# Kernel optimization log

Measured on AMD Instinct MI355X. Metric: run time of the kernel, lower is better.

Reference implementation:

```python
import jax, jax.numpy as jnp
import numpy as np

EPS = 1e-12  # matches torch F.normalize default eps

def _l2_normalize(x):
    # F.normalize: x / max(||x||, eps)
    n = jnp.linalg.norm(x, axis=-1, keepdims=True)
    return x / jnp.maximum(n, EPS)

def setup_inputs() -> dict:
    key = jax.random.key(0)
    k1, k2 = jax.random.split(key)
    sat = jax.random.normal(k1, (256, 64, 128), dtype=jnp.float32)   # [b, j, d]
    pano = jax.random.normal(k2, (64, 64, 128), dtype=jnp.float32)   # [a, i, d]
    return {"sat_embeddings_unnormalized": sat,
            "pano_embeddings_unnormalized": pano}

def reference(sat_embeddings_unnormalized, pano_embeddings_unnormalized):
    pano_n = _l2_normalize(pano_embeddings_unnormalized)  # [a, i, d]
    sat_n = _l2_normalize(sat_embeddings_unnormalized)    # [b, j, d]
    # similarity: [a, b, i, j]
    sim = jnp.einsum('aid,bjd->abij', pano_n, sat_n)
    # maxsim: max over sat tokens (j), sum over pano tokens (i) -> [a, b]
    return sim.max(axis=3).sum(axis=2)
```

## Files before the change

### kernel.cpp

```cpp
#include <hip/hip_runtime.h>
#include <hip/hip_bf16.h>


typedef __bf16 bf16x8 __attribute__((ext_vector_type(8)));
typedef float  f32x16 __attribute__((ext_vector_type(16)));
typedef unsigned int u32;

__device__ __forceinline__ void gload16(const void* g, void* l) {
    __builtin_amdgcn_global_load_lds((const __attribute__((address_space(1))) u32*)g,
                                     (__attribute__((address_space(3))) u32*)l, 16, 0, 0);
}

__device__ __forceinline__ unsigned short f2bf_rne(float x) {
    u32 u = __builtin_bit_cast(u32, x);
    return (unsigned short)((u + 0x7FFFu + ((u >> 16) & 1u)) >> 16);
}

__global__ __launch_bounds__(256) void normalize_all(
        const float* __restrict__ sat, const float* __restrict__ pano,
        unsigned short* __restrict__ satN, unsigned short* __restrict__ panoN) {
    int row  = blockIdx.x * 8 + (threadIdx.x >> 5);
    int lane = threadIdx.x & 31;
    const float* src;
    unsigned short* dst;
    if (row < 16384) { src = sat  + (size_t)row * 128;           dst = satN  + (size_t)row * 128; }
    else             { src = pano + (size_t)(row - 16384) * 128; dst = panoN + (size_t)(row - 16384) * 128; }
    const float4 v = *reinterpret_cast<const float4*>(src + lane * 4);
    float ss = v.x * v.x + v.y * v.y + v.z * v.z + v.w * v.w;
    #pragma unroll
    for (int m = 16; m >= 1; m >>= 1) ss += __shfl_xor(ss, m);
    float sc = 1.0f / fmaxf(sqrtf(ss), 1e-12f);
    ushort4 o;
    o.x = f2bf_rne(v.x * sc); o.y = f2bf_rne(v.y * sc);
    o.z = f2bf_rne(v.z * sc); o.w = f2bf_rne(v.w * sc);
    *reinterpret_cast<ushort4*>(dst + lane * 4) = o;
}

__global__ __launch_bounds__(256, 2) void maxsim_kernel(
        const unsigned short* __restrict__ satN,
        const unsigned short* __restrict__ panoN,
        float* __restrict__ out) {
    __shared__ unsigned short Slds[2][128 * 64];

    const int tid  = threadIdx.x;
    const int wid  = tid >> 6;
    const int lane = tid & 63;
    const int rl   = lane & 31;
    const int hi   = lane >> 5;

    const int bid = blockIdx.x;
    const int swz = (bid & 7) * 64 + (bid >> 3);
    const int jg  = swz >> 5;
    const int it  = swz & 31;

    const int wm = wid >> 1;
    const int wn = wid & 1;

    bf16x8 bfr[2][8];
    {
        const unsigned short* pb =
            panoN + ((size_t)(it * 128 + wn * 64 + rl)) * 128 + hi * 8;
        #pragma unroll
        for (int n = 0; n < 2; ++n)
            #pragma unroll
            for (int ks = 0; ks < 8; ++ks)
                bfr[n][ks] = *reinterpret_cast<const bf16x8*>(pb + (size_t)n * 32 * 128 + ks * 16);
    }

#define STAGE(t, kh) do {                                                      \
    const char* gb_ = (const char*)satN + ((size_t)(jg * 1024 + (t) * 128)) * 256 + (kh) * 128; \
    char* lb_ = (char*)&Slds[kh][0];                                           \
    _Pragma("unroll")                                                          \
    for (int i_ = 0; i_ < 4; ++i_) {                                           \
        int P_ = (wid * 4 + i_) * 1024 + lane * 16;                            \
        int r_ = P_ >> 7;                                                      \
        int g_ = ((P_ >> 4) & 7) ^ (r_ & 7);                                   \
        gload16(gb_ + (size_t)r_ * 256 + g_ * 16, lb_ + P_);                   \
    } } while (0)

#define COMPUTE(kh) do {                                                       \
    const char* sb_ = (const char*)&Slds[kh][0];                               \
    _Pragma("unroll")                                                          \
    for (int ks = 0; ks < 4; ++ks) {                                           \
        bf16x8 a_[2];                                                          \
        _Pragma("unroll")                                                      \
        for (int m = 0; m < 2; ++m) {                                          \
            int row = wm * 64 + m * 32 + rl;                                   \
            a_[m] = *(const bf16x8*)(sb_ + row * 128 + ((((ks << 1) | hi) ^ (row & 7)) << 4)); \
        }                                                                      \
        _Pragma("unroll")                                                      \
        for (int m = 0; m < 2; ++m)                                            \
            _Pragma("unroll")                                                  \
            for (int n = 0; n < 2; ++n)                                        \
                acc[m][n] = __builtin_amdgcn_mfma_f32_32x32x16_bf16(           \
                    a_[m], bfr[n][(kh) * 4 + ks], acc[m][n], 0, 0, 0);         \
    } } while (0)

    STAGE(0, 0);
    __syncthreads();

    #pragma unroll 1
    for (int t = 0; t < 8; ++t) {
        f32x16 acc[2][2] = {};

        STAGE(t, 1);
        __builtin_amdgcn_sched_barrier(0);
        COMPUTE(0);
        __syncthreads();

        if (t < 7) {
            STAGE(t + 1, 0);
            __builtin_amdgcn_sched_barrier(0);
        }
        COMPUTE(1);
        __syncthreads();

        float v0 = acc[0][0][0], v1 = acc[0][1][0];
        #pragma unroll
        for (int m = 0; m < 2; ++m)
            #pragma unroll
            for (int q = 0; q < 16; ++q) {
                if (m == 0 && q == 0) continue;
                v0 = fmaxf(v0, acc[m][0][q]);
                v1 = fmaxf(v1, acc[m][1][q]);
            }
        v0 = fmaxf(v0, __shfl_xor(v0, 32));
        v1 = fmaxf(v1, __shfl_xor(v1, 32));
        float s = v0 + v1;
        #pragma unroll
        for (int d = 1; d <= 16; d <<= 1) s += __shfl_xor(s, d);
        if (lane == 0) {
            int a = it * 2 + wn;
            int b = jg * 16 + t * 2 + wm;
            out[a * 256 + b] = s;
        }
    }
#undef STAGE
#undef COMPUTE
}

extern "C" void kernel_launch(void* const* d_in, const int* in_sizes, int n_in,
                              void* d_out, int out_size, void* d_ws, size_t ws_size,
                              hipStream_t stream) {
    const float* sat  = (const float*)d_in[0];
    const float* pano = (const float*)d_in[1];
    float* out = (float*)d_out;

    unsigned short* panoN = (unsigned short*)d_ws;
    unsigned short* satN  = panoN + (size_t)4096 * 128;

    normalize_all<<<2560, 256, 0, stream>>>(sat, pano, satN, panoN);
    maxsim_kernel<<<512, 256, 0, stream>>>(satN, panoN, out);
}
```

Before: 29.80 us.

## Deepen LDS pipeline to four buffers with partial vmcnt waits and setprio

Replaces the two-buffer LDS double-buffering with a four-slot ring that keeps three half-tiles in flight. Each step waits only on older loads via s_waitcnt vmcnt and a raw barrier instead of full __syncthreads. MFMA sections are wrapped in s_setprio. LDS doubles to 64KB per block, which may limit occupancy to two blocks per CU, and the hand-counted vmcnt values must match the number of loads issued per stage.

```diff
diff --git a/kernel.cpp b/kernel.cpp
--- a/kernel.cpp
+++ b/kernel.cpp
@@ -40,7 +40,7 @@
         const unsigned short* __restrict__ satN,
         const unsigned short* __restrict__ panoN,
         float* __restrict__ out) {
-    __shared__ unsigned short Slds[2][128 * 64];
+    __shared__ unsigned short Slds[4][128 * 64];
 
     const int tid  = threadIdx.x;
     const int wid  = tid >> 6;
@@ -67,76 +67,104 @@
                 bfr[n][ks] = *reinterpret_cast<const bf16x8*>(pb + (size_t)n * 32 * 128 + ks * 16);
     }
 
-#define STAGE(t, kh) do {                                                      \
-    const char* gb_ = (const char*)satN + ((size_t)(jg * 1024 + (t) * 128)) * 256 + (kh) * 128; \
-    char* lb_ = (char*)&Slds[kh][0];                                           \
-    _Pragma("unroll")                                                          \
-    for (int i_ = 0; i_ < 4; ++i_) {                                           \
-        int P_ = (wid * 4 + i_) * 1024 + lane * 16;                            \
-        int r_ = P_ >> 7;                                                      \
-        int g_ = ((P_ >> 4) & 7) ^ (r_ & 7);                                   \
-        gload16(gb_ + (size_t)r_ * 256 + g_ * 16, lb_ + P_);                   \
+#define STAGE(h_) do {                                                          \
+    const char* gb_ = (const char*)satN                                         \
+        + ((size_t)(jg * 1024 + ((h_) >> 1) * 128)) * 256 + ((h_) & 1) * 128;   \
+    char* lb_ = (char*)&Slds[(h_) & 3][0];                                      \
+    _Pragma("unroll")                                                           \
+    for (int i_ = 0; i_ < 4; ++i_) {                                            \
+        int P_ = (wid * 4 + i_) * 1024 + lane * 16;                             \
+        int r_ = P_ >> 7;                                                       \
+        int g_ = ((P_ >> 4) & 7) ^ (r_ & 7);                                    \
+        gload16(gb_ + (size_t)r_ * 256 + g_ * 16, lb_ + P_);                    \
     } } while (0)
 
-#define COMPUTE(kh) do {                                                       \
-    const char* sb_ = (const char*)&Slds[kh][0];                               \
-    _Pragma("unroll")                                                          \
-    for (int ks = 0; ks < 4; ++ks) {                                           \
-        bf16x8 a_[2];                                                          \
-        _Pragma("unroll")                                                      \
-        for (int m = 0; m < 2; ++m) {                                          \
-            int row = wm * 64 + m * 32 + rl;                                   \
+#define COMPUTE(h_, koff_) do {                                                 \
+    const char* sb_ = (const char*)&Slds[(h_) & 3][0];                          \
+    __builtin_amdgcn_s_setprio(1);                                              \
+    _Pragma("unroll")                                                           \
+    for (int ks = 0; ks < 4; ++ks) {                                            \
+        bf16x8 a_[2];                                                           \
+        _Pragma("unroll")                                                       \
+        for (int m = 0; m < 2; ++m) {                                           \
+            int row = wm * 64 + m * 32 + rl;                                    \
             a_[m] = *(const bf16x8*)(sb_ + row * 128 + ((((ks << 1) | hi) ^ (row & 7)) << 4)); \
-        }                                                                      \
-        _Pragma("unroll")                                                      \
-        for (int m = 0; m < 2; ++m)                                            \
-            _Pragma("unroll")                                                  \
-            for (int n = 0; n < 2; ++n)                                        \
-                acc[m][n] = __builtin_amdgcn_mfma_f32_32x32x16_bf16(           \
-                    a_[m], bfr[n][(kh) * 4 + ks], acc[m][n], 0, 0, 0);         \
-    } } while (0)
+        }                                                                       \
+        _Pragma("unroll")                                                       \
+        for (int m = 0; m < 2; ++m)                                             \
+            _Pragma("unroll")                                                   \
+            for (int n = 0; n < 2; ++n)                                         \
+                acc[m][n] = __builtin_amdgcn_mfma_f32_32x32x16_bf16(            \
+                    a_[m], bfr[n][(koff_) + ks], acc[m][n], 0, 0, 0);           \
+    }                                                                           \
+    __builtin_amdgcn_s_setprio(0);                                              \
+} while (0)
 
-    STAGE(0, 0);
-    __syncthreads();
+#define SYNC(N_) do {                                                           \
+    asm volatile("s_waitcnt vmcnt(" #N_ ")" ::: "memory");                      \
+    __builtin_amdgcn_s_barrier();                                               \
+    __builtin_amdgcn_sched_barrier(0);                                          \
+} while (0)
+
+#define EPILOGUE(t_) do {                                                       \
+    float v0 = acc[0][0][0], v1 = acc[0][1][0];                                 \
+    _Pragma("unroll")                                                           \
+    for (int m = 0; m < 2; ++m)                                                 \
+        _Pragma("unroll")                                                       \
+        for (int q = 0; q < 16; ++q) {                                          \
+            if (m == 0 && q == 0) continue;                                     \
+            v0 = fmaxf(v0, acc[m][0][q]);                                       \
+            v1 = fmaxf(v1, acc[m][1][q]);                                       \
+        }                                                                       \
+    v0 = fmaxf(v0, __shfl_xor(v0, 32));                                         \
+    v1 = fmaxf(v1, __shfl_xor(v1, 32));                                         \
+    float s_ = v0 + v1;                                                         \
+    _Pragma("unroll")                                                           \
+    for (int d_ = 1; d_ <= 16; d_ <<= 1) s_ += __shfl_xor(s_, d_);              \
+    if (lane == 0) out[(it * 2 + wn) * 256 + (jg * 16 + (t_) * 2 + wm)] = s_;   \
+    _Pragma("unroll")                                                           \
+    for (int m = 0; m < 2; ++m)                                                 \
+        _Pragma("unroll")                                                       \
+        for (int n = 0; n < 2; ++n)                                             \
+            _Pragma("unroll")                                                   \
+            for (int q = 0; q < 16; ++q) acc[m][n][q] = 0.f;                    \
+} while (0)
+
+    STAGE(0); STAGE(1); STAGE(2);
+
+    f32x16 acc[2][2];
+    #pragma unroll
+    for (int m = 0; m < 2; ++m)
+        #pragma unroll
+        for (int n = 0; n < 2; ++n)
+            #pragma unroll
+            for (int q = 0; q < 16; ++q) acc[m][n][q] = 0.f;
 
     #pragma unroll 1
-    for (int t = 0; t < 8; ++t) {
-        f32x16 acc[2][2] = {};
+    for (int t = 0; t < 7; ++t) {
+        const int h0 = 2 * t;
+        SYNC(8);
+        STAGE(h0 + 3);
+        __builtin_amdgcn_sched_barrier(0);
+        COMPUTE(h0, 0);
 
-        STAGE(t, 1);
+        SYNC(8);
+        if (t < 6) STAGE(h0 + 4);
         __builtin_amdgcn_sched_barrier(0);
-        COMPUTE(0);
-        __syncthreads();
+        COMPUTE(h0 + 1, 4);
 
-        if (t < 7) {
-            STAGE(t + 1, 0);
-            __builtin_amdgcn_sched_barrier(0);
-        }
-        COMPUTE(1);
-        __syncthreads();
+        EPILOGUE(t);
+    }
+    SYNC(4);
+    COMPUTE(14, 0);
+    SYNC(0);
+    COMPUTE(15, 4);
+    EPILOGUE(7);
 
-        float v0 = acc[0][0][0], v1 = acc[0][1][0];
-        #pragma unroll
-        for (int m = 0; m < 2; ++m)
-            #pragma unroll
-            for (int q = 0; q < 16; ++q) {
-                if (m == 0 && q == 0) continue;
-                v0 = fmaxf(v0, acc[m][0][q]);
-                v1 = fmaxf(v1, acc[m][1][q]);
-            }
-        v0 = fmaxf(v0, __shfl_xor(v0, 32));
-        v1 = fmaxf(v1, __shfl_xor(v1, 32));
-        float s = v0 + v1;
-        #pragma unroll
-        for (int d = 1; d <= 16; d <<= 1) s += __shfl_xor(s, d);
-        if (lane == 0) {
-            int a = it * 2 + wn;
-            int b = jg * 16 + t * 2 + wm;
-            out[a * 256 + b] = s;
-        }
-    }
 #undef STAGE
 #undef COMPUTE
+#undef SYNC
+#undef EPILOGUE
 }
 
 extern "C" void kernel_launch(void* const* d_in, const int* in_sizes, int n_in,
```

New measurement: 29.83 us. About the same (+0.1%).
